# Kernel tuning notes

Hardware: AMD Instinct MI355X
Metric: run time of the kernel (lower is better)

Reference implementation:

```python
import jax, jax.numpy as jnp
import numpy as np

NUM_RELS = 65
NUM_GRAPHS = 1500
NUM_MOTIFS = 6001  # row 0 dropped after scatter_mean
BN_EPS = 1e-5


def setup_inputs() -> dict:
    key = jax.random.key(0)
    ks = jax.random.split(key, 24)
    N, E, IN, H, FFN = 30000, 90000, 128, 128, 512
    p = lambda k, shp: jax.random.normal(k, shp, dtype=jnp.float32) * 0.05
    inp = {
        "node_feats": jax.random.normal(ks[0], (N, IN), dtype=jnp.float32),
        "src": jax.random.randint(ks[1], (E,), 0, N),
        "dst": jax.random.randint(ks[2], (E,), 0, N),
        "etype": jax.random.randint(ks[3], (E,), 0, NUM_RELS),
        "graph_ids": jnp.sort(jax.random.randint(ks[4], (N,), 0, NUM_GRAPHS)),
        "motif_batch": jax.random.randint(ks[5], (N,), 0, NUM_MOTIFS),
        # layer 1 params (in=128 -> out=128)
        "W1": p(ks[6], (NUM_RELS, IN, H)), "loopW1": p(ks[7], (IN, H)), "b1": jnp.zeros((H,), jnp.float32),
        "resW1": p(ks[8], (H, IN)), "resb1": jnp.zeros((H,), jnp.float32),
        "g1": jnp.ones((H,), jnp.float32), "be1": jnp.zeros((H,), jnp.float32),
        # layer 2 params (128 -> 128)
        "W2": p(ks[9], (NUM_RELS, H, H)), "loopW2": p(ks[10], (H, H)), "b2": jnp.zeros((H,), jnp.float32),
        "resW2": p(ks[11], (H, H)), "resb2": jnp.zeros((H,), jnp.float32),
        "g2": jnp.ones((H,), jnp.float32), "be2": jnp.zeros((H,), jnp.float32),
        # readout MLPs
        "feat_W": p(ks[12], (FFN, H)), "feat_b": jnp.zeros((FFN,), jnp.float32),
        "mlp_W1": p(ks[13], (FFN, FFN)), "mlp_b1": jnp.zeros((FFN,), jnp.float32),
        "mlp_W2": p(ks[14], (FFN // 2, FFN)), "mlp_b2": jnp.zeros((FFN // 2,), jnp.float32),
    }
    return inp


def _rgcn_layer(x, src, dst, etype, W, loopW, b, resW, resb, gamma, beta):
    # RelGraphConv with basis regularizer, num_bases == num_rels => per-relation weight.
    N = x.shape[0]
    # [R, N, out]: transform every node by every relation weight (one big GEMM)
    Hr = jnp.einsum('ni,rio->rno', x, W)
    msg = Hr[etype, src]                        # [E, out] gather per edge
    agg = jnp.zeros((N, W.shape[2]), x.dtype).at[dst].add(msg)  # sum aggregation
    h = agg + b + x @ loopW                     # bias + self loop
    h = jax.nn.relu(h)                          # conv activation (dropout=eval noop)
    res = jax.nn.relu(x @ resW.T + resb)        # residual branch
    h = h + res
    # BatchNorm1d, training-mode batch statistics (biased variance)
    mu = h.mean(axis=0)
    var = h.var(axis=0)
    return (h - mu) * jax.lax.rsqrt(var + BN_EPS) * gamma + beta


def _segment_mean(x, ids, num_segments):
    s = jax.ops.segment_sum(x, ids, num_segments=num_segments)
    cnt = jax.ops.segment_sum(jnp.ones((x.shape[0],), x.dtype), ids, num_segments=num_segments)
    return s / jnp.maximum(cnt, 1.0)[:, None]


def reference(node_feats, src, dst, etype, graph_ids, motif_batch,
              W1, loopW1, b1, resW1, resb1, g1, be1,
              W2, loopW2, b2, resW2, resb2, g2, be2,
              feat_W, feat_b, mlp_W1, mlp_b1, mlp_W2, mlp_b2):
    h = _rgcn_layer(node_feats, src, dst, etype, W1, loopW1, b1, resW1, resb1, g1, be1)
    h = _rgcn_layer(h, src, dst, etype, W2, loopW2, b2, resW2, resb2, g2, be2)

    def head(g):
        f = g @ feat_W.T + feat_b
        o = jax.nn.relu(f @ mlp_W1.T + mlp_b1)
        return o @ mlp_W2.T + mlp_b2

    graph_feats = _segment_mean(h, graph_ids, NUM_GRAPHS)      # AvgPooling readout
    out_global = head(graph_feats)
    h_sub = _segment_mean(h, motif_batch, NUM_MOTIFS)[1:, :]   # scatter_mean, drop row 0
    out_sub = head(h_sub)
    return graph_feats, out_global, out_sub
```

## Files before the change

### kernel.cpp

```cpp
#include <hip/hip_runtime.h>
#include <cstddef>

#define HD 128
#define NREL 65
#define NPB 32
#define SCB 1024
#define NTB ((2 * NREL + 2) * 16)

typedef __attribute__((ext_vector_type(8))) short bf16x8;
typedef __attribute__((ext_vector_type(4))) float f32x4;
#define MFMA_BF16(a, b, c) __builtin_amdgcn_mfma_f32_16x16x32_bf16(a, b, c, 0, 0, 0)

__device__ __forceinline__ unsigned short f2bf(float f) {
  unsigned int u = __float_as_uint(f);
  u += 0x7FFFu + ((u >> 16) & 1u);
  return (unsigned short)(u >> 16);
}
__device__ __forceinline__ float bf2f(unsigned short u) {
  return __uint_as_float((unsigned int)u << 16);
}
__device__ __forceinline__ float reluf(float v) { return v > 0.f ? v : 0.f; }

struct PrepArgs {
  const float* W1; const float* W2; const float* lw1; const float* lw2;
  unsigned short *W1t, *W2t, *l1t, *l2t;
  const float* csrc[6];
  unsigned short* cdst[6];
  int cn4[6];
  int total4;
};
__global__ void prep_all(PrepArgs a) {
  __shared__ float t[32][33];
  int b = blockIdx.x;
  if (b < NTB) {
    int z = b >> 4, tile = b & 15;
    const float* in; unsigned short* out;
    if (z < NREL)           { in = a.W1 + (size_t)z * HD * HD;          out = a.W1t + (size_t)z * HD * HD; }
    else if (z < 2 * NREL)  { in = a.W2 + (size_t)(z - NREL) * HD * HD; out = a.W2t + (size_t)(z - NREL) * HD * HD; }
    else if (z == 2 * NREL) { in = a.lw1; out = a.l1t; }
    else                    { in = a.lw2; out = a.l2t; }
    int k0 = (tile >> 2) * 32, n0 = (tile & 3) * 32;
    int tx = threadIdx.x & 31, ty = threadIdx.x >> 5;
#pragma unroll
    for (int it = 0; it < 4; ++it)
      t[ty + it * 8][tx] = in[(size_t)(k0 + ty + it * 8) * HD + n0 + tx];
    __syncthreads();
#pragma unroll
    for (int it = 0; it < 4; ++it)
      out[(size_t)(n0 + ty + it * 8) * HD + k0 + tx] = f2bf(t[tx][ty + it * 8]);
  } else {
    int i = (b - NTB) * 256 + threadIdx.x;
    if (i >= a.total4) return;
    int base = 0, s = -1, j = 0;
#pragma unroll
    for (int k = 0; k < 6; ++k) {
      if (s < 0 && i < base + a.cn4[k]) { s = k; j = i - base; }
      base += a.cn4[k];
    }
    float4 v = ((const float4*)a.csrc[s])[j];
    ushort4 o;
    o.x = f2bf(v.x); o.y = f2bf(v.y); o.z = f2bf(v.z); o.w = f2bf(v.w);
    ((ushort4*)a.cdst[s])[j] = o;
  }
}

__global__ void hist_all(const int* __restrict__ et, const int* __restrict__ dst,
                         const int* __restrict__ mid, int* __restrict__ rcounts,
                         int* __restrict__ dcount, int* __restrict__ mcount, int E, int N) {
  __shared__ int lc[NREL];
  int tid = threadIdx.x;
  if (tid < NREL) lc[tid] = 0;
  __syncthreads();
  int i = blockIdx.x * blockDim.x + tid;
  if (i < E) {
    atomicAdd(&lc[et[i]], 1);
    atomicAdd(&dcount[dst[i]], 1);
  } else if (i < E + N) {
    atomicAdd(&mcount[mid[i - E]], 1);
  }
  __syncthreads();
  if (tid < NREL && lc[tid] > 0) atomicAdd(&rcounts[tid], lc[tid]);
}

__global__ void rel_offsets(const int* __restrict__ counts, int* __restrict__ offs) {
  __shared__ int lc[NREL];
  int t = threadIdx.x;
  if (t < NREL) lc[t] = (counts[t] + 63) & ~63;
  __syncthreads();
  if (t <= NREL) {
    int o = 0;
    for (int r = 0; r < t; ++r) o += lc[r];
    offs[t] = o;
  }
}

__global__ void scan_blocks(const int* __restrict__ c0, int* __restrict__ o0, int* __restrict__ p0, int n0,
                            const int* __restrict__ c1, int* __restrict__ o1, int* __restrict__ p1, int n1) {
  int job = blockIdx.y;
  const int* cnt = job ? c1 : c0; int* offs = job ? o1 : o0; int* part = job ? p1 : p0;
  int n = job ? n1 : n0;
  int b = blockIdx.x;
  if (b * SCB >= n) return;
  __shared__ int t[SCB];
  int i = b * SCB + threadIdx.x;
  int v = (i < n) ? cnt[i] : 0;
  t[threadIdx.x] = v;
  __syncthreads();
  for (int d = 1; d < SCB; d <<= 1) {
    int x = (threadIdx.x >= d) ? t[threadIdx.x - d] : 0;
    __syncthreads();
    t[threadIdx.x] += x;
    __syncthreads();
  }
  if (i < n) offs[i] = t[threadIdx.x] - v;
  if (threadIdx.x == SCB - 1) part[b] = t[SCB - 1];
}

__global__ void scan_addback2(int* __restrict__ o0, const int* __restrict__ p0, int n0,
                              int* __restrict__ o1, const int* __restrict__ p1, int n1) {
  int job = blockIdx.y;
  int* o = job ? o1 : o0; const int* p = job ? p1 : p0; int n = job ? n1 : n0;
  __shared__ int pre;
  if (threadIdx.x == 0) {
    int s = 0;
    for (int b = 0; b < (int)blockIdx.x; ++b) s += p[b];
    pre = s;
  }
  __syncthreads();
  int i = blockIdx.x * SCB + threadIdx.x;
  if (i < n) o[i] += pre;
}

__global__ void scatter_all(const int* __restrict__ src, const int* __restrict__ dst,
                            const int* __restrict__ et, const int* __restrict__ mid,
                            const int* __restrict__ offs, int* __restrict__ cursor,
                            const int* __restrict__ doffs, int* __restrict__ dcursor,
                            const int* __restrict__ moffs, int* __restrict__ mcursor,
                            int* __restrict__ ssrc, int* __restrict__ chunk_rel,
                            int* __restrict__ sdpos, int* __restrict__ nidx, int E, int N) {
  __shared__ int lc[NREL];
  __shared__ int lbase[NREL];
  int tid = threadIdx.x;
  if (tid < NREL) lc[tid] = 0;
  __syncthreads();
  int i = blockIdx.x * blockDim.x + tid;
  int r = -1, lrank = 0;
  if (i < E) { r = et[i]; lrank = atomicAdd(&lc[r], 1); }
  __syncthreads();
  if (tid < NREL && lc[tid] > 0) lbase[tid] = atomicAdd(&cursor[tid], lc[tid]);
  __syncthreads();
  if (i < E) {
    int slot = offs[r] + lbase[r] + lrank;
    ssrc[slot] = src[i];
    chunk_rel[slot >> 6] = r;
    int d = dst[i];
    sdpos[slot] = doffs[d] + atomicAdd(&dcursor[d], 1);
  } else if (i < E + N) {
    int node = i - E;
    int m = mid[node];
    int mpos = moffs[m] + atomicAdd(&mcursor[m], 1);
    nidx[mpos] = node;
  }
}

__global__ __launch_bounds__(256, 8) void edge_gemm_msg(
    const unsigned short* __restrict__ xb, const unsigned short* __restrict__ Wt,
    const int* __restrict__ ssrc, const int* __restrict__ sdpos,
    const int* __restrict__ chunk_rel, unsigned short* __restrict__ msg) {
  int chunk = blockIdx.x;
  int rel = chunk_rel[chunk];
  if (rel < 0) return;
  int half = blockIdx.y;

  __shared__ __align__(16) unsigned short Ws[64][136];

  int tid = threadIdx.x;
  int lane = tid & 63, w = tid >> 6;
  int l15 = lane & 15, kg = lane >> 4;
  int base = chunk * 64;

  int srow = ssrc[base + w * 16 + l15];
  int dpos[4];
#pragma unroll
  for (int reg = 0; reg < 4; ++reg) dpos[reg] = sdpos[base + w * 16 + kg * 4 + reg];

  const unsigned short* Wr = Wt + (size_t)rel * HD * HD + (size_t)half * 64 * HD;
#pragma unroll
  for (int it = 0; it < 4; ++it) {
    int idx = it * 2048 + tid * 8;
    *(bf16x8*)&Ws[idx >> 7][idx & 127] = *(const bf16x8*)(Wr + idx);
  }

  bf16x8 afr[4];
  const bf16x8 zb = {0, 0, 0, 0, 0, 0, 0, 0};
  if (srow >= 0) {
    const unsigned short* xr = xb + (size_t)srow * HD + kg * 8;
#pragma unroll
    for (int t = 0; t < 4; ++t) afr[t] = *(const bf16x8*)(xr + t * 32);
  } else {
#pragma unroll
    for (int t = 0; t < 4; ++t) afr[t] = zb;
  }
  __syncthreads();

  f32x4 acc[4];
  const f32x4 zf = {0.f, 0.f, 0.f, 0.f};
#pragma unroll
  for (int c = 0; c < 4; ++c) acc[c] = zf;
#pragma unroll
  for (int t = 0; t < 4; ++t)
#pragma unroll
    for (int c = 0; c < 4; ++c) {
      bf16x8 bfr = *(const bf16x8*)&Ws[c * 16 + l15][t * 32 + kg * 8];
      acc[c] = MFMA_BF16(afr[t], bfr, acc[c]);
    }

#pragma unroll
  for (int reg = 0; reg < 4; ++reg) {
    if (dpos[reg] >= 0) {
      unsigned short* mp = msg + (size_t)dpos[reg] * HD + half * 64 + l15;
#pragma unroll
      for (int c = 0; c < 4; ++c) mp[c * 16] = f2bf(acc[c][reg]);
    }
  }
}

template<bool DUAL, int EPI, bool OBF16>
__global__ __launch_bounds__(256) void gemm_mfma(
    const unsigned short* __restrict__ A, const unsigned short* __restrict__ B1,
    const unsigned short* __restrict__ B2, const float* __restrict__ bias1,
    const float* __restrict__ bias2,
    const unsigned short* __restrict__ msgp, const int* __restrict__ gdoffs,
    const int* __restrict__ gdcount,
    float* __restrict__ Cf, unsigned short* __restrict__ Cb,
    float* __restrict__ colsum, int M, int N, int K) {
  __shared__ __align__(16) unsigned short As[64][40];
  __shared__ __align__(16) unsigned short B1s[64][40];
  __shared__ __align__(16) unsigned short B2s[DUAL ? 64 : 1][40];
  __shared__ float cs[2][64];

  int tid = threadIdx.x;
  int lane = tid & 63, w = tid >> 6;
  int wr = w >> 1, wc = w & 1;
  int l15 = lane & 15, kg = lane >> 4;
  int row0 = blockIdx.y * 64, col0 = blockIdx.x * 64;
  int srow = tid >> 2, skc = (tid & 3) * 8;

  f32x4 acc1[2][2], acc2[2][2];
  const f32x4 zf = {0.f, 0.f, 0.f, 0.f};
  const bf16x8 zb = {0, 0, 0, 0, 0, 0, 0, 0};
#pragma unroll
  for (int i = 0; i < 2; ++i)
#pragma unroll
    for (int j = 0; j < 2; ++j) { acc1[i][j] = zf; acc2[i][j] = zf; }

  for (int k0 = 0; k0 < K; k0 += 32) {
    {
      int gr = row0 + srow;
      bf16x8 v = zb;
      if (gr < M) v = *(const bf16x8*)(A + (size_t)gr * K + k0 + skc);
      *(bf16x8*)&As[srow][skc] = v;
      *(bf16x8*)&B1s[srow][skc] = *(const bf16x8*)(B1 + (size_t)(col0 + srow) * K + k0 + skc);
      if constexpr (DUAL)
        *(bf16x8*)&B2s[srow][skc] = *(const bf16x8*)(B2 + (size_t)(col0 + srow) * K + k0 + skc);
    }
    __syncthreads();
    bf16x8 af[2], b1f[2];
#pragma unroll
    for (int i = 0; i < 2; ++i) af[i] = *(const bf16x8*)&As[wr * 32 + i * 16 + l15][kg * 8];
#pragma unroll
    for (int j = 0; j < 2; ++j) b1f[j] = *(const bf16x8*)&B1s[wc * 32 + j * 16 + l15][kg * 8];
#pragma unroll
    for (int i = 0; i < 2; ++i)
#pragma unroll
      for (int j = 0; j < 2; ++j) acc1[i][j] = MFMA_BF16(af[i], b1f[j], acc1[i][j]);
    if constexpr (DUAL) {
      bf16x8 b2f[2];
#pragma unroll
      for (int j = 0; j < 2; ++j) b2f[j] = *(const bf16x8*)&B2s[wc * 32 + j * 16 + l15][kg * 8];
#pragma unroll
      for (int i = 0; i < 2; ++i)
#pragma unroll
        for (int j = 0; j < 2; ++j) acc2[i][j] = MFMA_BF16(af[i], b2f[j], acc2[i][j]);
    }
    __syncthreads();
  }

  float s[2] = {0.f, 0.f}, sq[2] = {0.f, 0.f};
#pragma unroll
  for (int i = 0; i < 2; ++i)
#pragma unroll
    for (int reg = 0; reg < 4; ++reg) {
      int row = row0 + wr * 32 + i * 16 + kg * 4 + reg;
      if (row < M) {
        float g[2] = {0.f, 0.f};
        if constexpr (EPI == 2) {
          int gb = gdoffs[row], gd = gdcount[row];
          const unsigned short* mp = msgp + (size_t)gb * HD + col0 + wc * 32 + l15;
          for (int e = 0; e < gd; ++e, mp += HD) {
            g[0] += bf2f(mp[0]);
            g[1] += bf2f(mp[16]);
          }
        }
#pragma unroll
        for (int j = 0; j < 2; ++j) {
          int col = col0 + wc * 32 + j * 16 + l15;
          float v = acc1[i][j][reg];
          if constexpr (EPI == 2) {
            v = reluf(v + bias1[col] + g[j]) + reluf(acc2[i][j][reg] + bias2[col]);
            Cf[(size_t)row * N + col] = v;
            s[j] += v; sq[j] += v * v;
          } else {
            v += bias1[col];
            if constexpr (EPI == 1) v = reluf(v);
            if constexpr (OBF16) Cb[(size_t)row * N + col] = f2bf(v);
            else Cf[(size_t)row * N + col] = v;
          }
        }
      }
    }
  if constexpr (EPI == 2) {
    __syncthreads();
    if (tid < 128) ((float*)cs)[tid] = 0.f;
    __syncthreads();
#pragma unroll
    for (int j = 0; j < 2; ++j) {
      int lc = wc * 32 + j * 16 + l15;
      atomicAdd(&cs[0][lc], s[j]);
      atomicAdd(&cs[1][lc], sq[j]);
    }
    __syncthreads();
    if (tid < 64) {
      atomicAdd(&colsum[col0 + tid], cs[0][tid]);
      atomicAdd(&colsum[HD + col0 + tid], cs[1][tid]);
    }
  }
}

__global__ void bn_apply_bf16(const float* __restrict__ h, unsigned short* __restrict__ hb,
                              const float* __restrict__ colsum, const float* __restrict__ gamma,
                              const float* __restrict__ beta, int M) {
  int i = blockIdx.x * blockDim.x + threadIdx.x;
  if (i >= M * (HD / 4)) return;
  int c0 = (i & 31) * 4;
  float invM = 1.f / (float)M;
  float4 v = ((const float4*)h)[i];
  float r[4] = {v.x, v.y, v.z, v.w};
#pragma unroll
  for (int j = 0; j < 4; ++j) {
    int c = c0 + j;
    float mu = colsum[c] * invM;
    float var = colsum[HD + c] * invM - mu * mu;
    r[j] = (r[j] - mu) * rsqrtf(var + 1e-5f) * gamma[c] + beta[c];
  }
  ushort4 o;
  o.x = f2bf(r[0]); o.y = f2bf(r[1]); o.z = f2bf(r[2]); o.w = f2bf(r[3]);
  ((ushort4*)hb)[i] = o;
}

__global__ __launch_bounds__(256) void seg_accum_g(
    const float* __restrict__ h, const int* __restrict__ gid,
    float* __restrict__ gsum, float* __restrict__ gcnt, int Nn) {
  int n0 = blockIdx.x * NPB;
  int half = threadIdx.x >> 7;
  int c = threadIdx.x & 127;
  float racc = 0.f; int rg = -1; int rlen = 0;
  for (int i = 0; i < NPB / 2; ++i) {
    int node = n0 + 2 * i + half;
    if (node >= Nn) break;
    float v = h[(size_t)node * HD + c];
    int g = gid[node];
    if (g != rg) {
      if (rg >= 0) {
        atomicAdd(&gsum[(size_t)rg * HD + c], racc);
        if (c == 0) atomicAdd(&gcnt[rg], (float)rlen);
      }
      rg = g; racc = v; rlen = 1;
    } else { racc += v; rlen++; }
  }
  if (rg >= 0) {
    atomicAdd(&gsum[(size_t)rg * HD + c], racc);
    if (c == 0) atomicAdd(&gcnt[rg], (float)rlen);
  }
}

__global__ __launch_bounds__(256) void readout_norm(
    const float* __restrict__ gsum, const float* __restrict__ gcnt,
    const float* __restrict__ h, const int* __restrict__ nidx,
    const int* __restrict__ moffs, const int* __restrict__ mcount,
    const float* __restrict__ colsum, const float* __restrict__ gamma,
    const float* __restrict__ beta, float invM,
    float* __restrict__ out_gf, unsigned short* __restrict__ headin, int NGr, int NMr) {
  int row = blockIdx.x * 2 + (threadIdx.x >> 7);
  if (row >= NGr + NMr) return;
  int c = threadIdx.x & 127;
  float mu = colsum[c] * invM;
  float var = colsum[HD + c] * invM - mu * mu;
  float sc = gamma[c] * rsqrtf(var + 1e-5f);
  float sh = beta[c] - mu * sc;
  if (row < NGr) {
    float n = gcnt[row];
    float v = (n > 0.f) ? (gsum[(size_t)row * HD + c] / n) * sc + sh : 0.f;
    out_gf[(size_t)row * HD + c] = v;
    headin[(size_t)row * HD + c] = f2bf(v);
  } else {
    int m = row - NGr;
    int deg = mcount[m], base = moffs[m];
    float acc = 0.f;
    for (int j = 0; j < deg; ++j) acc += h[(size_t)nidx[base + j] * HD + c];
    float v = (deg > 0) ? (acc / (float)deg) * sc + sh : 0.f;
    if (m > 0) headin[(size_t)(NGr + m - 1) * HD + c] = f2bf(v);
  }
}

extern "C" void kernel_launch(void* const* d_in, const int* in_sizes, int n_in,
                              void* d_out, int out_size, void* d_ws, size_t ws_size,
                              hipStream_t stream) {
  const float* x0     = (const float*)d_in[0];
  const int*   src    = (const int*)d_in[1];
  const int*   dst    = (const int*)d_in[2];
  const int*   etype  = (const int*)d_in[3];
  const int*   gids   = (const int*)d_in[4];
  const int*   mids   = (const int*)d_in[5];
  const float* W1     = (const float*)d_in[6];
  const float* loopW1 = (const float*)d_in[7];
  const float* b1     = (const float*)d_in[8];
  const float* resW1  = (const float*)d_in[9];
  const float* resb1  = (const float*)d_in[10];
  const float* g1     = (const float*)d_in[11];
  const float* be1    = (const float*)d_in[12];
  const float* W2     = (const float*)d_in[13];
  const float* loopW2 = (const float*)d_in[14];
  const float* b2     = (const float*)d_in[15];
  const float* resW2  = (const float*)d_in[16];
  const float* resb2  = (const float*)d_in[17];
  const float* g2     = (const float*)d_in[18];
  const float* be2    = (const float*)d_in[19];
  const float* featW  = (const float*)d_in[20];
  const float* featb  = (const float*)d_in[21];
  const float* mW1    = (const float*)d_in[22];
  const float* mb1    = (const float*)d_in[23];
  const float* mW2    = (const float*)d_in[24];
  const float* mb2    = (const float*)d_in[25];

  const int N = in_sizes[0] / HD;
  const int E = in_sizes[1];
  const int NG = 1500, NM = 6001, FFN = 512, OUT2 = 256;
  const int NCH = (E + 63) / 64 + NREL;
  const int NHD = N * HD;
  const int NHEAD = NG + NM - 1;

  float* ws = (float*)d_ws;
  size_t off = 0;
  auto alloc = [&](size_t n) { float* p = ws + off; off += (n + 63) & ~((size_t)63); return p; };
  float* hbuf  = alloc(NHD);
  unsigned short* msg = (unsigned short*)alloc((size_t)E * HD / 2);
  unsigned short* xb    = (unsigned short*)alloc(NHD / 2);
  unsigned short* W1tb  = (unsigned short*)alloc((size_t)NREL * HD * HD / 2);
  unsigned short* W2tb  = (unsigned short*)alloc((size_t)NREL * HD * HD / 2);
  unsigned short* lwT1b = (unsigned short*)alloc(HD * HD / 2);
  unsigned short* lwT2b = (unsigned short*)alloc(HD * HD / 2);
  unsigned short* rW1b  = (unsigned short*)alloc(HD * HD / 2);
  unsigned short* rW2b  = (unsigned short*)alloc(HD * HD / 2);
  unsigned short* featWb= (unsigned short*)alloc(FFN * HD / 2);
  unsigned short* mW1b  = (unsigned short*)alloc(FFN * FFN / 2);
  unsigned short* mW2b  = (unsigned short*)alloc(OUT2 * FFN / 2);
  unsigned short* headin= (unsigned short*)alloc((size_t)NHEAD * HD / 2);
  int* offs   = (int*)alloc(NREL + 1);
  int* doffs  = (int*)alloc(N);
  int* moffs  = (int*)alloc(NM);
  int* p0     = (int*)alloc(64);
  int* p1     = (int*)alloc(64);
  int* nidx   = (int*)alloc(N);
  size_t zero_start = off;
  int* counts  = (int*)alloc(NREL);
  int* cursor  = (int*)alloc(NREL);
  int* dcount  = (int*)alloc(N);
  int* dcursor = (int*)alloc(N);
  int* mcount  = (int*)alloc(NM);
  int* mcursor = (int*)alloc(NM);
  float* gsum  = alloc((size_t)NG * HD);
  float* gcnt  = alloc(NG);
  float* colsum1 = alloc(2 * HD);
  float* colsum2 = alloc(2 * HD);
  size_t zero_end = off;
  size_t ff_start = off;
  int* chunk_rel = (int*)alloc(NCH);
  int* ssrc      = (int*)alloc((size_t)NCH * 64);
  int* sdpos     = (int*)alloc((size_t)NCH * 64);
  size_t ff_end = off;
  unsigned short* fbuf_b = msg;
  unsigned short* obuf_b = msg + (size_t)NHEAD * FFN;

  float* out_gf = (float*)d_out;
  float* out_gl = out_gf + (size_t)NG * HD;

  dim3 blk(256);
  const int nb0 = (N + SCB - 1) / SCB;
  const int nb1 = (NM + SCB - 1) / SCB;

  PrepArgs pa{};
  pa.W1 = W1; pa.W2 = W2; pa.lw1 = loopW1; pa.lw2 = loopW2;
  pa.W1t = W1tb; pa.W2t = W2tb; pa.l1t = lwT1b; pa.l2t = lwT2b;
  pa.csrc[0] = x0;    pa.cdst[0] = xb;     pa.cn4[0] = NHD / 4;
  pa.csrc[1] = resW1; pa.cdst[1] = rW1b;   pa.cn4[1] = HD * HD / 4;
  pa.csrc[2] = resW2; pa.cdst[2] = rW2b;   pa.cn4[2] = HD * HD / 4;
  pa.csrc[3] = featW; pa.cdst[3] = featWb; pa.cn4[3] = FFN * HD / 4;
  pa.csrc[4] = mW1;   pa.cdst[4] = mW1b;   pa.cn4[4] = FFN * FFN / 4;
  pa.csrc[5] = mW2;   pa.cdst[5] = mW2b;   pa.cn4[5] = OUT2 * FFN / 4;
  pa.total4 = pa.cn4[0] + pa.cn4[1] + pa.cn4[2] + pa.cn4[3] + pa.cn4[4] + pa.cn4[5];
  int prepBlocks = NTB + (pa.total4 + 255) / 256;
  prep_all<<<prepBlocks, blk, 0, stream>>>(pa);

  hipMemsetAsync(ws + zero_start, 0, (zero_end - zero_start) * sizeof(float), stream);
  hipMemsetAsync(ws + ff_start, 0xFF, (ff_end - ff_start) * sizeof(float), stream);
  int histBlocks = (E + N + 255) / 256;
  hist_all<<<histBlocks, blk, 0, stream>>>(etype, dst, mids, counts, dcount, mcount, E, N);
  rel_offsets<<<1, 128, 0, stream>>>(counts, offs);
  scan_blocks<<<dim3(nb0, 2), SCB, 0, stream>>>(dcount, doffs, p0, N, mcount, moffs, p1, NM);
  scan_addback2<<<dim3(nb0, 2), SCB, 0, stream>>>(doffs, p0, N, moffs, p1, NM);
  scatter_all<<<histBlocks, blk, 0, stream>>>(src, dst, etype, mids, offs, cursor,
                                              doffs, dcursor, moffs, mcursor,
                                              ssrc, chunk_rel, sdpos, nidx, E, N);

  dim3 gridDual(HD / 64, (N + 63) / 64);
  dim3 gridEdge(NCH, 2);
  int bnBlocks = (N * (HD / 4) + 255) / 256;

  edge_gemm_msg<<<gridEdge, blk, 0, stream>>>(xb, W1tb, ssrc, sdpos, chunk_rel, msg);
  gemm_mfma<true, 2, false><<<gridDual, blk, 0, stream>>>(
      xb, lwT1b, rW1b, b1, resb1, msg, doffs, dcount, hbuf, nullptr, colsum1, N, HD, HD);
  bn_apply_bf16<<<bnBlocks, blk, 0, stream>>>(hbuf, xb, colsum1, g1, be1, N);

  edge_gemm_msg<<<gridEdge, blk, 0, stream>>>(xb, W2tb, ssrc, sdpos, chunk_rel, msg);
  gemm_mfma<true, 2, false><<<gridDual, blk, 0, stream>>>(
      xb, lwT2b, rW2b, b2, resb2, msg, doffs, dcount, hbuf, nullptr, colsum2, N, HD, HD);

  seg_accum_g<<<(N + NPB - 1) / NPB, blk, 0, stream>>>(hbuf, gids, gsum, gcnt, N);
  float invM = 1.f / (float)N;
  readout_norm<<<(NG + NM + 1) / 2, blk, 0, stream>>>(
      gsum, gcnt, hbuf, nidx, moffs, mcount, colsum2, g2, be2, invM, out_gf, headin, NG, NM);

  dim3 gA(FFN / 64, (NHEAD + 63) / 64);
  gemm_mfma<false, 0, true><<<gA, blk, 0, stream>>>(
      headin, featWb, nullptr, featb, nullptr, nullptr, nullptr, nullptr, nullptr, fbuf_b, nullptr, NHEAD, FFN, HD);
  gemm_mfma<false, 1, true><<<gA, blk, 0, stream>>>(
      fbuf_b, mW1b, nullptr, mb1, nullptr, nullptr, nullptr, nullptr, nullptr, obuf_b, nullptr, NHEAD, FFN, FFN);
  dim3 gC(OUT2 / 64, (NHEAD + 63) / 64);
  gemm_mfma<false, 0, false><<<gC, blk, 0, stream>>>(
      obuf_b, mW2b, nullptr, mb2, nullptr, nullptr, nullptr, nullptr, out_gl, nullptr, nullptr, NHEAD, OUT2, FFN);
}
```

Baseline: 215.3 us.

## Merge offset scans into one kernel and compute graph means from sorted ranges

Replaces the relation-offset, block-scan and add-back kernels with a single three-block scan kernel that does the relation offsets serially and the node and motif scans as per-thread chunked scans. Drops the atomic graph-sum accumulation kernel. Graph start indices are now derived from the sorted graph ids during scatter, and readout_norm sums each graph's contiguous node range directly. This removes several launches and the atomics on the gsum buffer. In exchange the scans run in only two blocks with serial per-thread chunks, and the graph readout loops sequentially over about 20 nodes per graph.

```diff
diff --git a/kernel.cpp b/kernel.cpp
--- a/kernel.cpp
+++ b/kernel.cpp
@@ -3,7 +3,6 @@
 
 #define HD 128
 #define NREL 65
-#define NPB 32
 #define SCB 1024
 #define NTB ((2 * NREL + 2) * 16)
 
@@ -82,62 +81,50 @@
   if (tid < NREL && lc[tid] > 0) atomicAdd(&rcounts[tid], lc[tid]);
 }
 
-__global__ void rel_offsets(const int* __restrict__ counts, int* __restrict__ offs) {
-  __shared__ int lc[NREL];
-  int t = threadIdx.x;
-  if (t < NREL) lc[t] = (counts[t] + 63) & ~63;
-  __syncthreads();
-  if (t <= NREL) {
-    int o = 0;
-    for (int r = 0; r < t; ++r) o += lc[r];
-    offs[t] = o;
-  }
-}
-
-__global__ void scan_blocks(const int* __restrict__ c0, int* __restrict__ o0, int* __restrict__ p0, int n0,
-                            const int* __restrict__ c1, int* __restrict__ o1, int* __restrict__ p1, int n1) {
-  int job = blockIdx.y;
-  const int* cnt = job ? c1 : c0; int* offs = job ? o1 : o0; int* part = job ? p1 : p0;
+__global__ void scan_all(const int* __restrict__ rcounts, int* __restrict__ roffs,
+                         const int* __restrict__ dcount, int* __restrict__ doffs, int n0,
+                         const int* __restrict__ mcount, int* __restrict__ moffs, int n1) {
+  int job = blockIdx.x;
+  if (job == 2) {
+    if (threadIdx.x == 0) {
+      int o = 0;
+      for (int r = 0; r < NREL; ++r) { roffs[r] = o; o += (rcounts[r] + 63) & ~63; }
+      roffs[NREL] = o;
+    }
+    return;
+  }
+  const int* cnt = job ? mcount : dcount;
+  int* o = job ? moffs : doffs;
   int n = job ? n1 : n0;
-  int b = blockIdx.x;
-  if (b * SCB >= n) return;
-  __shared__ int t[SCB];
-  int i = b * SCB + threadIdx.x;
-  int v = (i < n) ? cnt[i] : 0;
-  t[threadIdx.x] = v;
+  int CH = (n + SCB - 1) / SCB;
+  int t0 = threadIdx.x * CH;
+  int s = 0;
+  for (int k = 0; k < CH; ++k) { int idx = t0 + k; if (idx < n) s += cnt[idx]; }
+  __shared__ int tl[SCB];
+  tl[threadIdx.x] = s;
   __syncthreads();
   for (int d = 1; d < SCB; d <<= 1) {
-    int x = (threadIdx.x >= d) ? t[threadIdx.x - d] : 0;
-    __syncthreads();
-    t[threadIdx.x] += x;
-    __syncthreads();
-  }
-  if (i < n) offs[i] = t[threadIdx.x] - v;
-  if (threadIdx.x == SCB - 1) part[b] = t[SCB - 1];
-}
-
-__global__ void scan_addback2(int* __restrict__ o0, const int* __restrict__ p0, int n0,
-                              int* __restrict__ o1, const int* __restrict__ p1, int n1) {
-  int job = blockIdx.y;
-  int* o = job ? o1 : o0; const int* p = job ? p1 : p0; int n = job ? n1 : n0;
-  __shared__ int pre;
-  if (threadIdx.x == 0) {
-    int s = 0;
-    for (int b = 0; b < (int)blockIdx.x; ++b) s += p[b];
-    pre = s;
-  }
-  __syncthreads();
-  int i = blockIdx.x * SCB + threadIdx.x;
-  if (i < n) o[i] += pre;
+    int x = (threadIdx.x >= d) ? tl[threadIdx.x - d] : 0;
+    __syncthreads();
+    tl[threadIdx.x] += x;
+    __syncthreads();
+  }
+  int run = tl[threadIdx.x] - s;
+  for (int k = 0; k < CH; ++k) {
+    int idx = t0 + k;
+    if (idx < n) { o[idx] = run; run += cnt[idx]; }
+  }
 }
 
 __global__ void scatter_all(const int* __restrict__ src, const int* __restrict__ dst,
                             const int* __restrict__ et, const int* __restrict__ mid,
+                            const int* __restrict__ gid,
                             const int* __restrict__ offs, int* __restrict__ cursor,
                             const int* __restrict__ doffs, int* __restrict__ dcursor,
                             const int* __restrict__ moffs, int* __restrict__ mcursor,
                             int* __restrict__ ssrc, int* __restrict__ chunk_rel,
-                            int* __restrict__ sdpos, int* __restrict__ nidx, int E, int N) {
+                            int* __restrict__ sdpos, int* __restrict__ nidx,
+                            int* __restrict__ gstart, int E, int N, int NGc) {
   __shared__ int lc[NREL];
   __shared__ int lbase[NREL];
   int tid = threadIdx.x;
@@ -160,6 +147,11 @@
     int m = mid[node];
     int mpos = moffs[m] + atomicAdd(&mcursor[m], 1);
     nidx[mpos] = node;
+    int gcur = gid[node];
+    int gprev = (node == 0) ? -1 : gid[node - 1];
+    for (int g = gprev + 1; g <= gcur; ++g) gstart[g] = node;
+    if (node == N - 1)
+      for (int g = gcur + 1; g <= NGc; ++g) gstart[g] = N;
   }
 }
 
@@ -358,36 +350,10 @@
   ((ushort4*)hb)[i] = o;
 }
 
-__global__ __launch_bounds__(256) void seg_accum_g(
-    const float* __restrict__ h, const int* __restrict__ gid,
-    float* __restrict__ gsum, float* __restrict__ gcnt, int Nn) {
-  int n0 = blockIdx.x * NPB;
-  int half = threadIdx.x >> 7;
-  int c = threadIdx.x & 127;
-  float racc = 0.f; int rg = -1; int rlen = 0;
-  for (int i = 0; i < NPB / 2; ++i) {
-    int node = n0 + 2 * i + half;
-    if (node >= Nn) break;
-    float v = h[(size_t)node * HD + c];
-    int g = gid[node];
-    if (g != rg) {
-      if (rg >= 0) {
-        atomicAdd(&gsum[(size_t)rg * HD + c], racc);
-        if (c == 0) atomicAdd(&gcnt[rg], (float)rlen);
-      }
-      rg = g; racc = v; rlen = 1;
-    } else { racc += v; rlen++; }
-  }
-  if (rg >= 0) {
-    atomicAdd(&gsum[(size_t)rg * HD + c], racc);
-    if (c == 0) atomicAdd(&gcnt[rg], (float)rlen);
-  }
-}
-
 __global__ __launch_bounds__(256) void readout_norm(
-    const float* __restrict__ gsum, const float* __restrict__ gcnt,
-    const float* __restrict__ h, const int* __restrict__ nidx,
-    const int* __restrict__ moffs, const int* __restrict__ mcount,
+    const float* __restrict__ h, const int* __restrict__ gstart,
+    const int* __restrict__ nidx, const int* __restrict__ moffs,
+    const int* __restrict__ mcount,
     const float* __restrict__ colsum, const float* __restrict__ gamma,
     const float* __restrict__ beta, float invM,
     float* __restrict__ out_gf, unsigned short* __restrict__ headin, int NGr, int NMr) {
@@ -399,8 +365,10 @@
   float sc = gamma[c] * rsqrtf(var + 1e-5f);
   float sh = beta[c] - mu * sc;
   if (row < NGr) {
-    float n = gcnt[row];
-    float v = (n > 0.f) ? (gsum[(size_t)row * HD + c] / n) * sc + sh : 0.f;
+    int b = gstart[row], e2 = gstart[row + 1];
+    float acc = 0.f;
+    for (int n = b; n < e2; ++n) acc += h[(size_t)n * HD + c];
+    float v = (e2 > b) ? (acc / (float)(e2 - b)) * sc + sh : 0.f;
     out_gf[(size_t)row * HD + c] = v;
     headin[(size_t)row * HD + c] = f2bf(v);
   } else {
@@ -469,9 +437,8 @@
   int* offs   = (int*)alloc(NREL + 1);
   int* doffs  = (int*)alloc(N);
   int* moffs  = (int*)alloc(NM);
-  int* p0     = (int*)alloc(64);
-  int* p1     = (int*)alloc(64);
   int* nidx   = (int*)alloc(N);
+  int* gstart = (int*)alloc(NG + 1);
   size_t zero_start = off;
   int* counts  = (int*)alloc(NREL);
   int* cursor  = (int*)alloc(NREL);
@@ -479,8 +446,6 @@
   int* dcursor = (int*)alloc(N);
   int* mcount  = (int*)alloc(NM);
   int* mcursor = (int*)alloc(NM);
-  float* gsum  = alloc((size_t)NG * HD);
-  float* gcnt  = alloc(NG);
   float* colsum1 = alloc(2 * HD);
   float* colsum2 = alloc(2 * HD);
   size_t zero_end = off;
@@ -496,8 +461,6 @@
   float* out_gl = out_gf + (size_t)NG * HD;
 
   dim3 blk(256);
-  const int nb0 = (N + SCB - 1) / SCB;
-  const int nb1 = (NM + SCB - 1) / SCB;
 
   PrepArgs pa{};
   pa.W1 = W1; pa.W2 = W2; pa.lw1 = loopW1; pa.lw2 = loopW2;
@@ -516,12 +479,10 @@
   hipMemsetAsync(ws + ff_start, 0xFF, (ff_end - ff_start) * sizeof(float), stream);
   int histBlocks = (E + N + 255) / 256;
   hist_all<<<histBlocks, blk, 0, stream>>>(etype, dst, mids, counts, dcount, mcount, E, N);
-  rel_offsets<<<1, 128, 0, stream>>>(counts, offs);
-  scan_blocks<<<dim3(nb0, 2), SCB, 0, stream>>>(dcount, doffs, p0, N, mcount, moffs, p1, NM);
-  scan_addback2<<<dim3(nb0, 2), SCB, 0, stream>>>(doffs, p0, N, moffs, p1, NM);
-  scatter_all<<<histBlocks, blk, 0, stream>>>(src, dst, etype, mids, offs, cursor,
+  scan_all<<<3, SCB, 0, stream>>>(counts, offs, dcount, doffs, N, mcount, moffs, NM);
+  scatter_all<<<histBlocks, blk, 0, stream>>>(src, dst, etype, mids, gids, offs, cursor,
                                               doffs, dcursor, moffs, mcursor,
-                                              ssrc, chunk_rel, sdpos, nidx, E, N);
+                                              ssrc, chunk_rel, sdpos, nidx, gstart, E, N, NG);
 
   dim3 gridDual(HD / 64, (N + 63) / 64);
   dim3 gridEdge(NCH, 2);
@@ -536,10 +497,9 @@
   gemm_mfma<true, 2, false><<<gridDual, blk, 0, stream>>>(
       xb, lwT2b, rW2b, b2, resb2, msg, doffs, dcount, hbuf, nullptr, colsum2, N, HD, HD);
 
-  seg_accum_g<<<(N + NPB - 1) / NPB, blk, 0, stream>>>(hbuf, gids, gsum, gcnt, N);
   float invM = 1.f / (float)N;
   readout_norm<<<(NG + NM + 1) / 2, blk, 0, stream>>>(
-      gsum, gcnt, hbuf, nidx, moffs, mcount, colsum2, g2, be2, invM, out_gf, headin, NG, NM);
+      hbuf, gstart, nidx, moffs, mcount, colsum2, g2, be2, invM, out_gf, headin, NG, NM);
 
   dim3 gA(FFN / 64, (NHEAD + 63) / 64);
   gemm_mfma<false, 0, true><<<gA, blk, 0, stream>>>(
```

New measurement: 247.9 us. +15.1%, slower.
